# Kernel optimization log

Measured on AMD Instinct MI355X. Metric: run time of the kernel, lower is better.

The kernel has to match this reference:

```python
import jax, jax.numpy as jnp
import numpy as np

D_MODEL = 1024
N_HEADS = 16
HEAD_DIM = D_MODEL // N_HEADS


def setup_inputs() -> dict:
    key = jax.random.key(0)
    k_x, k_wqkv, k_bqkv, k_wo, k_bo = jax.random.split(key, 5)
    b, t = 4, 2048
    s = 1.0 / np.sqrt(D_MODEL)
    return {
        "x": jax.random.normal(k_x, (b, t, D_MODEL), dtype=jnp.float32),
        "w_qkv": jax.random.uniform(k_wqkv, (D_MODEL, 3 * D_MODEL), jnp.float32, -s, s),
        "b_qkv": jax.random.uniform(k_bqkv, (3 * D_MODEL,), jnp.float32, -s, s),
        "w_out": jax.random.uniform(k_wo, (D_MODEL, D_MODEL), jnp.float32, -s, s),
        "b_out": jax.random.uniform(k_bo, (D_MODEL,), jnp.float32, -s, s),
    }


def reference(x, w_qkv, b_qkv, w_out, b_out):
    b, t, _ = x.shape
    # fused QKV projection -> [b, t, 3, h, d] -> q,k,v each [b, h, t, d]
    qkv = (x @ w_qkv + b_qkv).reshape(b, t, 3, N_HEADS, HEAD_DIM)
    q, k, v = jnp.moveaxis(qkv, 2, 0)          # each [b, t, h, d]
    q = q.transpose(0, 2, 1, 3)                # [b, h, t, d]
    k = k.transpose(0, 2, 1, 3)
    v = v.transpose(0, 2, 1, 3)
    scale = 1.0 / np.sqrt(HEAD_DIM).astype(np.float32)
    logits = jnp.einsum('bhqd,bhkd->bhqk', q, k) * scale
    causal = jnp.tril(jnp.ones((t, t), dtype=bool))
    logits = jnp.where(causal, logits, jnp.finfo(logits.dtype).min)
    attn = jax.nn.softmax(logits, axis=-1)
    out = jnp.einsum('bhqk,bhkd->bhqd', attn, v)      # [b, h, t, d]
    out = out.transpose(0, 2, 1, 3).reshape(b, t, D_MODEL)
    return out @ w_out + b_out
```

## Files before the change

### kernel.cpp

```cpp
#include <hip/hip_runtime.h>
#include <hip/hip_bf16.h>
#include <math.h>

#define NHEADS 16
#define HDIM   64
#define SEQT   2048
#define NBATCH 4
#define DMODEL 1024
#define MROWS  (NBATCH * SEQT)

typedef __bf16 bf16;
typedef bf16  bf16x8 __attribute__((ext_vector_type(8)));
typedef float f32x4  __attribute__((ext_vector_type(4)));
typedef float f32x16 __attribute__((ext_vector_type(16)));
typedef unsigned int u32x4 __attribute__((ext_vector_type(4)));

#define MFMA_BF16(a, b, c) __builtin_amdgcn_mfma_f32_16x16x32_bf16((a), (b), (c), 0, 0, 0)
#define MFMA32(a, b, c)    __builtin_amdgcn_mfma_f32_32x32x16_bf16((a), (b), (c), 0, 0, 0)
#define Z16 {0.f,0.f,0.f,0.f,0.f,0.f,0.f,0.f,0.f,0.f,0.f,0.f,0.f,0.f,0.f,0.f}

__device__ __forceinline__ void gload_lds16(const void* g, void* l) {
  __builtin_amdgcn_global_load_lds((const __attribute__((address_space(1))) void*)g,
                                   (__attribute__((address_space(3))) void*)l, 16, 0, 0);
}

__device__ __forceinline__ unsigned cvtpk_bf16(float lo, float hi) {
  unsigned r;
  asm("v_cvt_pk_bf16_f32 %0, %1, %2" : "=v"(r) : "v"(lo), "v"(hi));
  return r;
}
__device__ __forceinline__ void plswap(unsigned& a, unsigned& b) {
  asm volatile("v_permlane32_swap_b32 %0, %1" : "+v"(a), "+v"(b));
}


__global__ __launch_bounds__(256) void k_cvt_f32_bf16(const float* __restrict__ in,
                                                      bf16* __restrict__ out, int n8) {
  int i = blockIdx.x * blockDim.x + threadIdx.x;
  if (i >= n8) return;
  const float4* in4 = (const float4*)in;
  float4 a = in4[(size_t)i * 2], b = in4[(size_t)i * 2 + 1];
  bf16x8 v;
  v[0] = (bf16)a.x; v[1] = (bf16)a.y; v[2] = (bf16)a.z; v[3] = (bf16)a.w;
  v[4] = (bf16)b.x; v[5] = (bf16)b.y; v[6] = (bf16)b.z; v[7] = (bf16)b.w;
  *(bf16x8*)(out + (size_t)i * 8) = v;
}

__global__ __launch_bounds__(256) void k_transpose_f32_bf16(const float* __restrict__ in,
                                                            bf16* __restrict__ out,
                                                            int R, int C) {
  int nct = C >> 6;
  int rt = blockIdx.x / nct, ct = blockIdx.x % nct;
  __shared__ float tile[64][65];
  int tid = threadIdx.x;
#pragma unroll
  for (int i = 0; i < 16; i++) {
    int e = i * 256 + tid, r = e >> 6, c = e & 63;
    tile[r][c] = in[(size_t)(rt * 64 + r) * C + ct * 64 + c];
  }
  __syncthreads();
#pragma unroll
  for (int i = 0; i < 16; i++) {
    int e = i * 256 + tid, r = e >> 6, c = e & 63;
    out[(size_t)(ct * 64 + r) * R + rt * 64 + c] = (bf16)tile[c][r];
  }
}

__global__ __launch_bounds__(256) void k_transpose_v(const bf16* __restrict__ v,
                                                     bf16* __restrict__ vt) {
  int tt = blockIdx.x & 31;
  int bh = blockIdx.x >> 5;
  __shared__ bf16 tile[64][65];
  int tid = threadIdx.x;
  const bf16* src = v + (size_t)bh * SEQT * 64 + (size_t)tt * 64 * 64;
#pragma unroll
  for (int i = 0; i < 16; i++) {
    int e = i * 256 + tid, r = e >> 6, c = e & 63;
    tile[r][c] = src[r * 64 + c];
  }
  __syncthreads();
  bf16* dst = vt + (size_t)bh * 64 * SEQT + tt * 64;
#pragma unroll
  for (int i = 0; i < 16; i++) {
    int e = i * 256 + tid, r = e >> 6, c = e & 63;
    dst[(size_t)r * SEQT + c] = tile[c][r];
  }
}


__device__ __forceinline__ void gemm128_core(const bf16* __restrict__ A,
                                             const bf16* __restrict__ Bt,
                                             int K, int bm, int bn, char* smem,
                                             f32x4 (&acc)[4][4]) {
  int tid = threadIdx.x, lane = tid & 63, w = tid >> 6;
  int l15 = lane & 15, g = lane >> 4;
  int wrow = (w >> 1) * 64, wcol = (w & 1) * 64;
  char* As = smem;
  char* Bs = smem + 8192;
  const char* Ag = (const char*)(A + (size_t)bm * 128 * K);
  const char* Bg = (const char*)(Bt + (size_t)bn * 128 * K);
  const int rowB = K * 2;
  int srow = w * 16 + (lane >> 2);
  int scol = (lane & 3) * 16;

  for (int kt = 0; kt < K / 32; kt++) {
#pragma unroll
    for (int is = 0; is < 2; is++) {
      int row = is * 64 + srow;
      gload_lds16(Ag + (size_t)row * rowB + kt * 64 + scol, As + is * 4096 + w * 1024);
      gload_lds16(Bg + (size_t)row * rowB + kt * 64 + scol, Bs + is * 4096 + w * 1024);
    }
    __syncthreads();
    bf16x8 af[4], bfr[4];
#pragma unroll
    for (int i = 0; i < 4; i++)
      af[i] = *(const bf16x8*)&As[(wrow + i * 16 + l15) * 64 + g * 16];
#pragma unroll
    for (int j = 0; j < 4; j++)
      bfr[j] = *(const bf16x8*)&Bs[(wcol + j * 16 + l15) * 64 + g * 16];
#pragma unroll
    for (int i = 0; i < 4; i++)
#pragma unroll
      for (int j = 0; j < 4; j++)
        acc[i][j] = MFMA_BF16(af[i], bfr[j], acc[i][j]);
    __syncthreads();
  }
}

__global__ __launch_bounds__(256) void k_gemm_qkv(const bf16* __restrict__ A,
                                                  const bf16* __restrict__ Bt,
                                                  const float* __restrict__ bias,
                                                  bf16* __restrict__ Qo,
                                                  bf16* __restrict__ Ko,
                                                  bf16* __restrict__ Vo) {
  const int K = DMODEL, NB = 24;
  int bm = blockIdx.x / NB, bn = blockIdx.x % NB;
  __shared__ __align__(16) char smem[16384];
  f32x4 acc[4][4] = {};
  gemm128_core(A, Bt, K, bm, bn, smem, acc);

  int tid = threadIdx.x, lane = tid & 63, w = tid >> 6;
  int l15 = lane & 15, g = lane >> 4;
  int wrow = (w >> 1) * 64, wcol = (w & 1) * 64;
  int rowbase = bm * 128 + wrow;
  int b = (bm * 128) >> 11;
#pragma unroll
  for (int j = 0; j < 4; j++) {
    int n = bn * 128 + wcol + j * 16 + l15;
    float bj = bias[n];
    int which = n >> 10;
    int nn = n & 1023;
    int head = nn >> 6, d = nn & 63;
    bf16* dst = (which == 0) ? Qo : (which == 1) ? Ko : Vo;
    size_t base = ((size_t)(b * NHEADS + head) * SEQT) * 64 + d;
#pragma unroll
    for (int i = 0; i < 4; i++) {
#pragma unroll
      for (int r = 0; r < 4; r++) {
        int row = rowbase + i * 16 + g * 4 + r;
        int t = row & (SEQT - 1);
        dst[base + (size_t)t * 64] = (bf16)(acc[i][j][r] + bj);
      }
    }
  }
}

__global__ __launch_bounds__(256) void k_gemm_out(const bf16* __restrict__ A,
                                                  const bf16* __restrict__ Bt,
                                                  const float* __restrict__ bias,
                                                  float* __restrict__ C) {
  const int K = DMODEL, NB = 8;
  int bm = blockIdx.x / NB, bn = blockIdx.x % NB;
  __shared__ __align__(16) char smem[16384];
  f32x4 acc[4][4] = {};
  gemm128_core(A, Bt, K, bm, bn, smem, acc);

  int tid = threadIdx.x, lane = tid & 63, w = tid >> 6;
  int l15 = lane & 15, g = lane >> 4;
  int wrow = (w >> 1) * 64, wcol = (w & 1) * 64;
#pragma unroll
  for (int j = 0; j < 4; j++) {
    int n = bn * 128 + wcol + j * 16 + l15;
    float bj = bias[n];
#pragma unroll
    for (int i = 0; i < 4; i++) {
#pragma unroll
      for (int r = 0; r < 4; r++) {
        int row = bm * 128 + wrow + i * 16 + g * 4 + r;
        C[(size_t)row * DMODEL + n] = acc[i][j][r] + bj;
      }
    }
  }
}


__global__ __launch_bounds__(256) void k_attn(const bf16* __restrict__ Q,
                                              const bf16* __restrict__ Kg,
                                              const bf16* __restrict__ VT,
                                              bf16* __restrict__ Oo) {
  int bh = blockIdx.x & 63;
  int qi = 15 - (blockIdx.x >> 6);
  int tid = threadIdx.x, lane = tid & 63, wv = tid >> 6;
  int l31 = lane & 31, hi = lane >> 5;
  __shared__ __align__(16) char smem[32768];

  const bf16* Qbh = Q + (size_t)bh * SEQT * 64;
  const char* Kbyte = (const char*)(Kg + (size_t)bh * SEQT * 64);
  const char* Vbyte = (const char*)(VT + (size_t)bh * 64 * SEQT);
  int qbase = qi * 128 + wv * 32;
  int ql = qbase + l31;

  int pA = tid * 16, pB = pA + 4096;
  int rA = pA >> 7, rB = pB >> 7;
  int lgA = pA ^ ((rA & 7) << 4), lgB = pB ^ ((rB & 7) << 4);
  int vA = rA * 4096 + (lgA & 127), vB = rB * 4096 + (lgB & 127);

  bf16x8 qf[4];
#pragma unroll
  for (int s = 0; s < 4; s++) {
    bf16x8 v = *(const bf16x8*)(Qbh + (size_t)ql * 64 + s * 16 + hi * 8);
#pragma unroll
    for (int e = 0; e < 8; e++) v[e] = (bf16)((float)v[e] * 0.125f);
    qf[s] = v;
  }

  float m = -INFINITY, lsum = 0.f;
  f32x16 o[2] = {Z16, Z16};

  gload_lds16(Kbyte + lgA, smem + pA);
  gload_lds16(Kbyte + lgB, smem + pB);
  gload_lds16(Vbyte + vA, smem + 16384 + pA);
  gload_lds16(Vbyte + vB, smem + 16384 + pB);

  int NT = 2 * qi + 2, cur = 0;
  for (int j = 0; j < NT; j++) {
    __syncthreads();
    if (j + 1 < NT) {
      int nx = cur ^ 1;
      const char* kg = Kbyte + (size_t)(j + 1) * 8192;
      const char* vg = Vbyte + (size_t)(j + 1) * 128;
      gload_lds16(kg + lgA, smem + nx * 8192 + pA);
      gload_lds16(kg + lgB, smem + nx * 8192 + pB);
      gload_lds16(vg + vA, smem + 16384 + nx * 8192 + pA);
      gload_lds16(vg + vB, smem + 16384 + nx * 8192 + pB);
    }
    if (j * 64 <= qbase + 31) {
      const char* Ks = smem + cur * 8192;
      const char* Vs = smem + 16384 + cur * 8192;

      f32x16 st[2];
#pragma unroll
      for (int h = 0; h < 2; h++) {
        f32x16 acc = Z16;
#pragma unroll
        for (int s = 0; s < 4; s++) {
          int row = h * 32 + l31;
          bf16x8 kf = *(const bf16x8*)&Ks[(row * 128 + s * 32 + hi * 16) ^ ((l31 & 7) << 4)];
          acc = MFMA32(kf, qf[s], acc);
        }
        st[h] = acc;
      }

      if (j * 64 + 63 > qbase) {
        int rel = ql - (j * 64 + 4 * hi);
#pragma unroll
        for (int r = 0; r < 16; r++) {
          const int R0 = (r & 3) + 8 * (r >> 2);
          if (R0 > rel) st[0][r] = -INFINITY;
          if (R0 > rel - 32) st[1][r] = -INFINITY;
        }
      }

      float m0 = -INFINITY, m1 = -INFINITY, m2 = -INFINITY, m3 = -INFINITY;
#pragma unroll
      for (int h = 0; h < 2; h++)
#pragma unroll
        for (int r = 0; r < 16; r += 4) {
          m0 = fmaxf(m0, st[h][r]);
          m1 = fmaxf(m1, st[h][r + 1]);
          m2 = fmaxf(m2, st[h][r + 2]);
          m3 = fmaxf(m3, st[h][r + 3]);
        }
      float mx = fmaxf(fmaxf(m0, m1), fmaxf(m2, m3));
      mx = fmaxf(mx, __shfl_xor(mx, 32));

      if (__any(mx > m + 8.f)) {
        float mn = fmaxf(m, mx), co = __expf(m - mn);
        m = mn; lsum *= co;
#pragma unroll
        for (int r = 0; r < 16; r++) {
          const int R0 = (r & 3) + 8 * (r >> 2);
          float fac = __shfl(co, R0 + 4 * hi);
          o[0][r] *= fac; o[1][r] *= fac;
        }
      }

      float s0 = 0.f, s1 = 0.f, s2 = 0.f, s3 = 0.f;
#pragma unroll
      for (int h = 0; h < 2; h++)
#pragma unroll
        for (int r = 0; r < 16; r += 4) {
          float p0 = __expf(st[h][r] - m);     st[h][r] = p0;     s0 += p0;
          float p1 = __expf(st[h][r + 1] - m); st[h][r + 1] = p1; s1 += p1;
          float p2 = __expf(st[h][r + 2] - m); st[h][r + 2] = p2; s2 += p2;
          float p3 = __expf(st[h][r + 3] - m); st[h][r + 3] = p3; s3 += p3;
        }
      lsum += (s0 + s1) + (s2 + s3);

#pragma unroll
      for (int h = 0; h < 2; h++) {
        unsigned pw[8];
#pragma unroll
        for (int i = 0; i < 8; i++) pw[i] = cvtpk_bf16(st[h][2 * i], st[h][2 * i + 1]);
        plswap(pw[0], pw[2]); plswap(pw[1], pw[3]);
        plswap(pw[4], pw[6]); plswap(pw[5], pw[7]);
        u32x4 f0 = {pw[0], pw[1], pw[2], pw[3]};
        u32x4 f1 = {pw[4], pw[5], pw[6], pw[7]};
        bf16x8 pa0 = __builtin_bit_cast(bf16x8, f0);
        bf16x8 pa1 = __builtin_bit_cast(bf16x8, f1);
#pragma unroll
        for (int dh = 0; dh < 2; dh++) {
          int vrow = dh * 32 + l31;
          bf16x8 bv0 = *(const bf16x8*)&Vs[(vrow * 128 + (2 * h) * 32 + hi * 16) ^ ((l31 & 7) << 4)];
          bf16x8 bv1 = *(const bf16x8*)&Vs[(vrow * 128 + (2 * h + 1) * 32 + hi * 16) ^ ((l31 & 7) << 4)];
          o[dh] = MFMA32(pa0, bv0, o[dh]);
          o[dh] = MFMA32(pa1, bv1, o[dh]);
        }
      }
    }
    cur ^= 1;
  }

  float inv = 1.f / (lsum + __shfl_xor(lsum, 32));
  int b = bh >> 4, hd = bh & 15;
#pragma unroll
  for (int r = 0; r < 16; r++) {
    const int R0 = (r & 3) + 8 * (r >> 2);
    float fac = __shfl(inv, R0 + 4 * hi);
    int qrow = qbase + R0 + 4 * hi;
    size_t off = ((size_t)(b * SEQT + qrow)) * DMODEL + hd * 64;
    Oo[off + l31]      = (bf16)(o[0][r] * fac);
    Oo[off + 32 + l31] = (bf16)(o[1][r] * fac);
  }
}


extern "C" void kernel_launch(void* const* d_in, const int* in_sizes, int n_in,
                              void* d_out, int out_size, void* d_ws, size_t ws_size,
                              hipStream_t stream) {
  const float* x     = (const float*)d_in[0];
  const float* w_qkv = (const float*)d_in[1];
  const float* b_qkv = (const float*)d_in[2];
  const float* w_out = (const float*)d_in[3];
  const float* b_out = (const float*)d_in[4];
  float* out = (float*)d_out;

  char* ws = (char*)d_ws;
  bf16* xb    = (bf16*)(ws);
  bf16* wqkvT = (bf16*)(ws + (16u << 20));
  bf16* woutT = (bf16*)(ws + (22u << 20));
  bf16* Qb    = (bf16*)(ws + (24u << 20));
  bf16* Kb    = (bf16*)(ws + (40u << 20));
  bf16* Vb    = (bf16*)(ws + (56u << 20));
  bf16* VTb   = (bf16*)(ws + (72u << 20));
  bf16* attn_o = xb;

  k_cvt_f32_bf16<<<(MROWS * DMODEL / 8 + 255) / 256, 256, 0, stream>>>(x, xb, MROWS * DMODEL / 8);
  k_transpose_f32_bf16<<<16 * 48, 256, 0, stream>>>(w_qkv, wqkvT, DMODEL, 3 * DMODEL);
  k_transpose_f32_bf16<<<16 * 16, 256, 0, stream>>>(w_out, woutT, DMODEL, DMODEL);
  k_gemm_qkv<<<64 * 24, 256, 0, stream>>>(xb, wqkvT, b_qkv, Qb, Kb, Vb);
  k_transpose_v<<<64 * 32, 256, 0, stream>>>(Vb, VTb);
  k_attn<<<16 * 64, 256, 0, stream>>>(Qb, Kb, VTb, attn_o);
  k_gemm_out<<<64 * 8, 256, 0, stream>>>(attn_o, woutT, b_out, out);
}
```

Before: 261.7 us.

## Shrink attention blocks, compute row sums by MFMA, add setprio and block swizzle

The attention kernel now runs 128-thread blocks covering 64 query rows each, with twice as many blocks. Each block now handles the causal diagonal only on its last tile, which removes the per-wave skip logic. Row sums of the softmax probabilities are accumulated with an MFMA against a ones vector instead of scalar adds. Exponentials use native exp2 with a fused log2e scale. Both GEMMs remap block IDs with an XCD-style swizzle, and all MFMA sections get s_setprio raised to favour matrix issue. Smaller blocks give finer load balance on the causal triangle but mean less K/V reuse per block, and the ones-MFMA adds matrix work.

```diff
diff --git a/kernel.cpp b/kernel.cpp
--- a/kernel.cpp
+++ b/kernel.cpp
@@ -18,6 +18,7 @@
 #define MFMA_BF16(a, b, c) __builtin_amdgcn_mfma_f32_16x16x32_bf16((a), (b), (c), 0, 0, 0)
 #define MFMA32(a, b, c)    __builtin_amdgcn_mfma_f32_32x32x16_bf16((a), (b), (c), 0, 0, 0)
 #define Z16 {0.f,0.f,0.f,0.f,0.f,0.f,0.f,0.f,0.f,0.f,0.f,0.f,0.f,0.f,0.f,0.f}
+#define LOG2E 1.44269504f
 
 __device__ __forceinline__ void gload_lds16(const void* g, void* l) {
   __builtin_amdgcn_global_load_lds((const __attribute__((address_space(1))) void*)g,
@@ -31,6 +32,11 @@
 }
 __device__ __forceinline__ void plswap(unsigned& a, unsigned& b) {
   asm volatile("v_permlane32_swap_b32 %0, %1" : "+v"(a), "+v"(b));
+}
+__device__ __forceinline__ float exp2v(float x) {
+  float r;
+  asm("v_exp_f32 %0, %1" : "=v"(r) : "v"(x));
+  return r;
 }
 
 
@@ -118,11 +124,13 @@
 #pragma unroll
     for (int j = 0; j < 4; j++)
       bfr[j] = *(const bf16x8*)&Bs[(wcol + j * 16 + l15) * 64 + g * 16];
+    __builtin_amdgcn_s_setprio(1);
 #pragma unroll
     for (int i = 0; i < 4; i++)
 #pragma unroll
       for (int j = 0; j < 4; j++)
         acc[i][j] = MFMA_BF16(af[i], bfr[j], acc[i][j]);
+    __builtin_amdgcn_s_setprio(0);
     __syncthreads();
   }
 }
@@ -134,7 +142,8 @@
                                                   bf16* __restrict__ Ko,
                                                   bf16* __restrict__ Vo) {
   const int K = DMODEL, NB = 24;
-  int bm = blockIdx.x / NB, bn = blockIdx.x % NB;
+  int bid = (blockIdx.x & 7) * 192 + (blockIdx.x >> 3);
+  int bm = bid / NB, bn = bid % NB;
   __shared__ __align__(16) char smem[16384];
   f32x4 acc[4][4] = {};
   gemm128_core(A, Bt, K, bm, bn, smem, acc);
@@ -170,7 +179,8 @@
                                                   const float* __restrict__ bias,
                                                   float* __restrict__ C) {
   const int K = DMODEL, NB = 8;
-  int bm = blockIdx.x / NB, bn = blockIdx.x % NB;
+  int bid = (blockIdx.x & 7) * 64 + (blockIdx.x >> 3);
+  int bm = bid / NB, bn = bid % NB;
   __shared__ __align__(16) char smem[16384];
   f32x4 acc[4][4] = {};
   gemm128_core(A, Bt, K, bm, bn, smem, acc);
@@ -194,12 +204,12 @@
 }
 
 
-__global__ __launch_bounds__(256) void k_attn(const bf16* __restrict__ Q,
+__global__ __launch_bounds__(128) void k_attn(const bf16* __restrict__ Q,
                                               const bf16* __restrict__ Kg,
                                               const bf16* __restrict__ VT,
                                               bf16* __restrict__ Oo) {
   int bh = blockIdx.x & 63;
-  int qi = 15 - (blockIdx.x >> 6);
+  int qi = 31 - (blockIdx.x >> 6);
   int tid = threadIdx.x, lane = tid & 63, wv = tid >> 6;
   int l31 = lane & 31, hi = lane >> 5;
   __shared__ __align__(16) char smem[32768];
@@ -207,13 +217,18 @@
   const bf16* Qbh = Q + (size_t)bh * SEQT * 64;
   const char* Kbyte = (const char*)(Kg + (size_t)bh * SEQT * 64);
   const char* Vbyte = (const char*)(VT + (size_t)bh * 64 * SEQT);
-  int qbase = qi * 128 + wv * 32;
+  int qbase = qi * 64 + wv * 32;
   int ql = qbase + l31;
 
-  int pA = tid * 16, pB = pA + 4096;
-  int rA = pA >> 7, rB = pB >> 7;
-  int lgA = pA ^ ((rA & 7) << 4), lgB = pB ^ ((rB & 7) << 4);
-  int vA = rA * 4096 + (lgA & 127), vB = rB * 4096 + (lgB & 127);
+  int pp[4], lgK[4]; size_t vOff[4];
+#pragma unroll
+  for (int c = 0; c < 4; c++) {
+    int p = c * 2048 + tid * 16;
+    int row = p >> 7;
+    int lg = p ^ ((row & 7) << 4);
+    pp[c] = p; lgK[c] = lg;
+    vOff[c] = (size_t)row * (SEQT * 2) + (lg & 127);
+  }
 
   bf16x8 qf[4];
 #pragma unroll
@@ -224,123 +239,133 @@
     qf[s] = v;
   }
 
-  float m = -INFINITY, lsum = 0.f;
-  f32x16 o[2] = {Z16, Z16};
-
-  gload_lds16(Kbyte + lgA, smem + pA);
-  gload_lds16(Kbyte + lgB, smem + pB);
-  gload_lds16(Vbyte + vA, smem + 16384 + pA);
-  gload_lds16(Vbyte + vB, smem + 16384 + pB);
-
-  int NT = 2 * qi + 2, cur = 0;
-  for (int j = 0; j < NT; j++) {
+  bf16x8 onesf;
+#pragma unroll
+  for (int e = 0; e < 8; e++) onesf[e] = (bf16)1.0f;
+
+  float m = -INFINITY;
+  f32x16 o0 = Z16, o1 = Z16, lacc = Z16;
+
+#pragma unroll
+  for (int c = 0; c < 4; c++) {
+    gload_lds16(Kbyte + lgK[c], smem + pp[c]);
+    gload_lds16(Vbyte + vOff[c], smem + 16384 + pp[c]);
+  }
+
+  int NT = qi + 1;
+  for (int t = 0; t < NT; t++) {
     __syncthreads();
-    if (j + 1 < NT) {
-      int nx = cur ^ 1;
-      const char* kg = Kbyte + (size_t)(j + 1) * 8192;
-      const char* vg = Vbyte + (size_t)(j + 1) * 128;
-      gload_lds16(kg + lgA, smem + nx * 8192 + pA);
-      gload_lds16(kg + lgB, smem + nx * 8192 + pB);
-      gload_lds16(vg + vA, smem + 16384 + nx * 8192 + pA);
-      gload_lds16(vg + vB, smem + 16384 + nx * 8192 + pB);
-    }
-    if (j * 64 <= qbase + 31) {
-      const char* Ks = smem + cur * 8192;
-      const char* Vs = smem + 16384 + cur * 8192;
-
-      f32x16 st[2];
-#pragma unroll
-      for (int h = 0; h < 2; h++) {
-        f32x16 acc = Z16;
-#pragma unroll
-        for (int s = 0; s < 4; s++) {
-          int row = h * 32 + l31;
-          bf16x8 kf = *(const bf16x8*)&Ks[(row * 128 + s * 32 + hi * 16) ^ ((l31 & 7) << 4)];
-          acc = MFMA32(kf, qf[s], acc);
-        }
-        st[h] = acc;
-      }
-
-      if (j * 64 + 63 > qbase) {
-        int rel = ql - (j * 64 + 4 * hi);
-#pragma unroll
-        for (int r = 0; r < 16; r++) {
-          const int R0 = (r & 3) + 8 * (r >> 2);
-          if (R0 > rel) st[0][r] = -INFINITY;
-          if (R0 > rel - 32) st[1][r] = -INFINITY;
-        }
-      }
-
-      float m0 = -INFINITY, m1 = -INFINITY, m2 = -INFINITY, m3 = -INFINITY;
-#pragma unroll
-      for (int h = 0; h < 2; h++)
-#pragma unroll
-        for (int r = 0; r < 16; r += 4) {
-          m0 = fmaxf(m0, st[h][r]);
-          m1 = fmaxf(m1, st[h][r + 1]);
-          m2 = fmaxf(m2, st[h][r + 2]);
-          m3 = fmaxf(m3, st[h][r + 3]);
-        }
-      float mx = fmaxf(fmaxf(m0, m1), fmaxf(m2, m3));
-      mx = fmaxf(mx, __shfl_xor(mx, 32));
-
-      if (__any(mx > m + 8.f)) {
-        float mn = fmaxf(m, mx), co = __expf(m - mn);
-        m = mn; lsum *= co;
-#pragma unroll
-        for (int r = 0; r < 16; r++) {
-          const int R0 = (r & 3) + 8 * (r >> 2);
-          float fac = __shfl(co, R0 + 4 * hi);
-          o[0][r] *= fac; o[1][r] *= fac;
-        }
-      }
-
-      float s0 = 0.f, s1 = 0.f, s2 = 0.f, s3 = 0.f;
-#pragma unroll
-      for (int h = 0; h < 2; h++)
-#pragma unroll
-        for (int r = 0; r < 16; r += 4) {
-          float p0 = __expf(st[h][r] - m);     st[h][r] = p0;     s0 += p0;
-          float p1 = __expf(st[h][r + 1] - m); st[h][r + 1] = p1; s1 += p1;
-          float p2 = __expf(st[h][r + 2] - m); st[h][r + 2] = p2; s2 += p2;
-          float p3 = __expf(st[h][r + 3] - m); st[h][r + 3] = p3; s3 += p3;
-        }
-      lsum += (s0 + s1) + (s2 + s3);
-
-#pragma unroll
-      for (int h = 0; h < 2; h++) {
-        unsigned pw[8];
-#pragma unroll
-        for (int i = 0; i < 8; i++) pw[i] = cvtpk_bf16(st[h][2 * i], st[h][2 * i + 1]);
-        plswap(pw[0], pw[2]); plswap(pw[1], pw[3]);
-        plswap(pw[4], pw[6]); plswap(pw[5], pw[7]);
-        u32x4 f0 = {pw[0], pw[1], pw[2], pw[3]};
-        u32x4 f1 = {pw[4], pw[5], pw[6], pw[7]};
-        bf16x8 pa0 = __builtin_bit_cast(bf16x8, f0);
-        bf16x8 pa1 = __builtin_bit_cast(bf16x8, f1);
-#pragma unroll
-        for (int dh = 0; dh < 2; dh++) {
-          int vrow = dh * 32 + l31;
-          bf16x8 bv0 = *(const bf16x8*)&Vs[(vrow * 128 + (2 * h) * 32 + hi * 16) ^ ((l31 & 7) << 4)];
-          bf16x8 bv1 = *(const bf16x8*)&Vs[(vrow * 128 + (2 * h + 1) * 32 + hi * 16) ^ ((l31 & 7) << 4)];
-          o[dh] = MFMA32(pa0, bv0, o[dh]);
-          o[dh] = MFMA32(pa1, bv1, o[dh]);
-        }
-      }
-    }
-    cur ^= 1;
-  }
-
-  float inv = 1.f / (lsum + __shfl_xor(lsum, 32));
+    if (t + 1 < NT) {
+      int nx = (t + 1) & 1;
+      const char* kg = Kbyte + (size_t)(t + 1) * 8192;
+      const char* vg = Vbyte + (size_t)(t + 1) * 128;
+#pragma unroll
+      for (int c = 0; c < 4; c++) {
+        gload_lds16(kg + lgK[c], smem + nx * 8192 + pp[c]);
+        gload_lds16(vg + vOff[c], smem + 16384 + nx * 8192 + pp[c]);
+      }
+    }
+    const char* Ks = smem + (t & 1) * 8192;
+    const char* Vs = smem + 16384 + (t & 1) * 8192;
+
+    f32x16 st[2];
+    __builtin_amdgcn_s_setprio(1);
+#pragma unroll
+    for (int h = 0; h < 2; h++) {
+      f32x16 acc = Z16;
+#pragma unroll
+      for (int s = 0; s < 4; s++) {
+        int row = h * 32 + l31;
+        bf16x8 kf = *(const bf16x8*)&Ks[(row * 128 + s * 32 + hi * 16) ^ ((l31 & 7) << 4)];
+        acc = MFMA32(kf, qf[s], acc);
+      }
+      st[h] = acc;
+    }
+    __builtin_amdgcn_s_setprio(0);
+
+    if (t == NT - 1) {
+      int rel = ql - (t * 64 + 4 * hi);
+#pragma unroll
+      for (int r = 0; r < 16; r++) {
+        const int R0 = (r & 3) + 8 * (r >> 2);
+        if (R0 > rel) st[0][r] = -INFINITY;
+        if (R0 > rel - 32) st[1][r] = -INFINITY;
+      }
+    }
+
+    float m0 = -INFINITY, m1 = -INFINITY, m2 = -INFINITY, m3 = -INFINITY;
+#pragma unroll
+    for (int h = 0; h < 2; h++)
+#pragma unroll
+      for (int r = 0; r < 16; r += 4) {
+        m0 = fmaxf(m0, st[h][r]);
+        m1 = fmaxf(m1, st[h][r + 1]);
+        m2 = fmaxf(m2, st[h][r + 2]);
+        m3 = fmaxf(m3, st[h][r + 3]);
+      }
+    float mx = fmaxf(fmaxf(m0, m1), fmaxf(m2, m3));
+    mx = fmaxf(mx, __shfl_xor(mx, 32));
+
+    if (__any(mx > m + 8.f)) {
+      float mn = fmaxf(m, mx);
+      float co = exp2v((m - mn) * LOG2E);
+      m = mn;
+#pragma unroll
+      for (int r = 0; r < 16; r++) {
+        const int R0 = (r & 3) + 8 * (r >> 2);
+        float fac = __shfl(co, R0 + 4 * hi);
+        o0[r] *= fac; o1[r] *= fac; lacc[r] *= fac;
+      }
+    }
+
+    float negmq = -m * LOG2E;
+#pragma unroll
+    for (int h = 0; h < 2; h++)
+#pragma unroll
+      for (int r = 0; r < 16; r++)
+        st[h][r] = exp2v(fmaf(st[h][r], LOG2E, negmq));
+
+    __builtin_amdgcn_s_setprio(1);
+#pragma unroll
+    for (int h = 0; h < 2; h++) {
+      unsigned pw[8];
+#pragma unroll
+      for (int i = 0; i < 8; i++) pw[i] = cvtpk_bf16(st[h][2 * i], st[h][2 * i + 1]);
+      plswap(pw[0], pw[2]); plswap(pw[1], pw[3]);
+      plswap(pw[4], pw[6]); plswap(pw[5], pw[7]);
+      u32x4 f0 = {pw[0], pw[1], pw[2], pw[3]};
+      u32x4 f1 = {pw[4], pw[5], pw[6], pw[7]};
+      bf16x8 pa0 = __builtin_bit_cast(bf16x8, f0);
+      bf16x8 pa1 = __builtin_bit_cast(bf16x8, f1);
+      lacc = MFMA32(pa0, onesf, lacc);
+      lacc = MFMA32(pa1, onesf, lacc);
+      {
+        int vrow = l31;
+        bf16x8 bv0 = *(const bf16x8*)&Vs[(vrow * 128 + (2 * h) * 32 + hi * 16) ^ ((l31 & 7) << 4)];
+        bf16x8 bv1 = *(const bf16x8*)&Vs[(vrow * 128 + (2 * h + 1) * 32 + hi * 16) ^ ((l31 & 7) << 4)];
+        o0 = MFMA32(pa0, bv0, o0);
+        o0 = MFMA32(pa1, bv1, o0);
+      }
+      {
+        int vrow = 32 + l31;
+        bf16x8 bv0 = *(const bf16x8*)&Vs[(vrow * 128 + (2 * h) * 32 + hi * 16) ^ ((l31 & 7) << 4)];
+        bf16x8 bv1 = *(const bf16x8*)&Vs[(vrow * 128 + (2 * h + 1) * 32 + hi * 16) ^ ((l31 & 7) << 4)];
+        o1 = MFMA32(pa0, bv0, o1);
+        o1 = MFMA32(pa1, bv1, o1);
+      }
+    }
+    __builtin_amdgcn_s_setprio(0);
+  }
+
   int b = bh >> 4, hd = bh & 15;
 #pragma unroll
   for (int r = 0; r < 16; r++) {
     const int R0 = (r & 3) + 8 * (r >> 2);
-    float fac = __shfl(inv, R0 + 4 * hi);
     int qrow = qbase + R0 + 4 * hi;
+    float inv = 1.f / lacc[r];
     size_t off = ((size_t)(b * SEQT + qrow)) * DMODEL + hd * 64;
-    Oo[off + l31]      = (bf16)(o[0][r] * fac);
-    Oo[off + 32 + l31] = (bf16)(o[1][r] * fac);
+    Oo[off + l31]      = (bf16)(o0[r] * inv);
+    Oo[off + 32 + l31] = (bf16)(o1[r] * inv);
   }
 }
 
@@ -370,6 +395,6 @@
   k_transpose_f32_bf16<<<16 * 16, 256, 0, stream>>>(w_out, woutT, DMODEL, DMODEL);
   k_gemm_qkv<<<64 * 24, 256, 0, stream>>>(xb, wqkvT, b_qkv, Qb, Kb, Vb);
   k_transpose_v<<<64 * 32, 256, 0, stream>>>(Vb, VTb);
-  k_attn<<<16 * 64, 256, 0, stream>>>(Qb, Kb, VTb, attn_o);
+  k_attn<<<32 * 64, 128, 0, stream>>>(Qb, Kb, VTb, attn_o);
   k_gemm_out<<<64 * 8, 256, 0, stream>>>(attn_o, woutT, b_out, out);
 }
```

Measured after the change: 268.7 us. 1.03x slower.
